# Optimization experiments

Measured on AMD Instinct MI355X. Metric: run time of the kernel, lower is better.

## Reference

```python
import jax, jax.numpy as jnp
import numpy as np
from jax import lax

B, L, D = 2, 2048, 128
H, HD = 8, 32
WIN = 3

def setup_inputs() -> dict:
    key = jax.random.key(0)
    ks = jax.random.split(key, 7)
    s = 0.05
    return {
        "x":  jax.random.normal(ks[0], (B, L, D), jnp.float32),
        "pe": jax.random.normal(ks[1], (L, D), jnp.float32) * s,
        "Wq": jax.random.normal(ks[2], (D, H * HD), jnp.float32) * s,
        "bq": jnp.zeros((H * HD,), jnp.float32),
        "Wk": jax.random.normal(ks[3], (D, H * HD), jnp.float32) * s,
        "bk": jnp.zeros((H * HD,), jnp.float32),
        "Wv": jax.random.normal(ks[4], (D, H), jnp.float32) * s,
    }

def reference(x, pe, Wq, bq, Wk, bk, Wv):
    b, l, d = x.shape
    h = Wv.shape[1]
    hd = Wq.shape[1] // h
    xp = x + pe                                   # (B,L,D)
    # split heads: Dense output columns [i*hd:(i+1)*hd] -> head i
    q = (xp @ Wq + bq).reshape(b, l, h, hd).transpose(2, 0, 1, 3)  # (H,B,L,hd)
    k = (xp @ Wk + bk).reshape(b, l, h, hd).transpose(2, 0, 1, 3)  # (H,B,L,hd)
    v = jax.nn.sigmoid(x @ Wv).transpose(2, 0, 1)                  # (H,B,L)

    attn = jnp.einsum('hbqd,hbkd->hbqk', q, k) * (float(hd) ** -0.5)
    attn = jax.nn.softmax(attn, axis=-1)          # (H,B,L,L)

    # band_part(0,-1) + diag_part(k=(0,L-1)) (RIGHT_LEFT align) + transpose + reverse(-2,-1)
    # collapses to the skew-gather: R[p, m] = attn[L-1-p-m, L-1-p] for p+m <= L-1 else 0
    p = jnp.arange(l)[:, None]                    # (L,1)
    m = jnp.arange(l)[None, :]                    # (1,L)
    ii = l - 1 - p - m                            # row index  (L,L)
    jj = jnp.broadcast_to(l - 1 - p, (l, l))      # col index  (L,L)
    valid = (ii >= 0)
    R = attn[:, :, jnp.where(valid, ii, 0), jj] * valid.astype(attn.dtype)  # (H,B,L,L)

    R = R * v[:, :, :, None]                      # gate by value, broadcast over distance axis

    # TF avg_pool excludes padding from the divisor
    sums = lax.reduce_window(R, 0.0, lax.add, (1, 1, 1, WIN), (1, 1, 1, 1), 'SAME')
    cnt = lax.reduce_window(jnp.ones((l,), R.dtype), 0.0, lax.add, (WIN,), (1,), 'SAME')
    pooled = sums / cnt                           # (H,B,L,L)

    # global mode: sum over position axis, -> (B, L_dist, H)
    out = pooled.sum(axis=2).transpose(1, 2, 0)
    return out
```

## Files before the change

### kernel.cpp

```cpp
#include <hip/hip_runtime.h>
#include <hip/hip_bf16.h>

#define LSEQ 2048
#define BB 2
#define DD 128
#define HH 8
#define HD 32

#define FPSCALE 524288.0f
#define RFPSCALE (1.0f / 524288.0f)
#define QSCALE 0.25503486f

typedef __bf16 bf8_t __attribute__((ext_vector_type(8)));
typedef __bf16 bf4_t __attribute__((ext_vector_type(4)));
typedef float f4_t __attribute__((ext_vector_type(4)));

static __device__ __forceinline__ float fexp2(float x) {
#if __has_builtin(__builtin_amdgcn_exp2f)
    return __builtin_amdgcn_exp2f(x);
#else
    float r;
    asm("v_exp_f32 %0, %1" : "=v"(r) : "v"(x));
    return r;
#endif
}

__global__ __launch_bounds__(256) void k_A(const float* __restrict__ x,
                                           const float* __restrict__ pe,
                                           const float* __restrict__ Wq,
                                           const float* __restrict__ Wk,
                                           const float* __restrict__ Wv,
                                           const float* __restrict__ bq,
                                           const float* __restrict__ bk,
                                           float* __restrict__ w,
                                           __bf16* __restrict__ Qb,
                                           __bf16* __restrict__ Kb,
                                           int* __restrict__ Si) {
    __shared__ __align__(16) char smem[34816];
    int gb = blockIdx.x;
    int tid = threadIdx.x;

    if (gb < 512) {
        __bf16* xs = (__bf16*)smem;
        __bf16* Wt = (__bf16*)(smem + 64 * 136 * 2);
        int jr = gb >> 3, y = gb & 7;
        int row0 = jr * 64;
        bool isK = y >= 4;
        int cbase = (y & 3) * 64;
        const float* W = isK ? Wk : Wq;

        #pragma unroll
        for (int i = 0; i < 8; i++) {
            int idx4 = tid + i * 256;
            int row = idx4 >> 5, col4 = idx4 & 31;
            float4 xv = ((const float4*)x)[row0 * 32 + idx4];
            float4 pv = ((const float4*)pe)[((row0 + row) & (LSEQ - 1)) * 32 + col4];
            bf4_t o = {(__bf16)(xv.x + pv.x), (__bf16)(xv.y + pv.y),
                       (__bf16)(xv.z + pv.z), (__bf16)(xv.w + pv.w)};
            *(bf4_t*)&xs[row * 136 + col4 * 4] = o;
        }
        #pragma unroll
        for (int i = 0; i < 8; i++) {
            int idx4 = tid + i * 256;
            int d = idx4 >> 4, c4 = (idx4 & 15) * 4;
            float4 wv4 = *(const float4*)(W + d * 256 + cbase + c4);
            Wt[(c4 + 0) * 136 + d] = (__bf16)wv4.x;
            Wt[(c4 + 1) * 136 + d] = (__bf16)wv4.y;
            Wt[(c4 + 2) * 136 + d] = (__bf16)wv4.z;
            Wt[(c4 + 3) * 136 + d] = (__bf16)wv4.w;
        }
        __syncthreads();

        int wid = tid >> 6, lane = tid & 63;
        int lm = lane & 15, lq = lane >> 4;
        int c0loc = wid * 16;
        f4_t acc0 = {0,0,0,0}, acc1 = {0,0,0,0}, acc2 = {0,0,0,0}, acc3 = {0,0,0,0};
        #pragma unroll
        for (int s = 0; s < 4; s++) {
            bf8_t bw = *(const bf8_t*)&Wt[(c0loc + lm) * 136 + lq * 8 + s * 32];
            bf8_t a0 = *(const bf8_t*)&xs[(0  + lm) * 136 + lq * 8 + s * 32];
            bf8_t a1 = *(const bf8_t*)&xs[(16 + lm) * 136 + lq * 8 + s * 32];
            bf8_t a2 = *(const bf8_t*)&xs[(32 + lm) * 136 + lq * 8 + s * 32];
            bf8_t a3 = *(const bf8_t*)&xs[(48 + lm) * 136 + lq * 8 + s * 32];
            acc0 = __builtin_amdgcn_mfma_f32_16x16x32_bf16(a0, bw, acc0, 0, 0, 0);
            acc1 = __builtin_amdgcn_mfma_f32_16x16x32_bf16(a1, bw, acc1, 0, 0, 0);
            acc2 = __builtin_amdgcn_mfma_f32_16x16x32_bf16(a2, bw, acc2, 0, 0, 0);
            acc3 = __builtin_amdgcn_mfma_f32_16x16x32_bf16(a3, bw, acc3, 0, 0, 0);
        }
        int c = cbase + c0loc + lm;
        float bv = (isK ? bk : bq)[c];
        float qs = isK ? 1.f : QSCALE;
        __bf16* Out = isK ? Kb : Qb;
        int h = c >> 5, hd = c & 31;
        f4_t accs[4] = {acc0, acc1, acc2, acc3};
        #pragma unroll
        for (int rs = 0; rs < 4; rs++) {
            #pragma unroll
            for (int r = 0; r < 4; r++) {
                int row = row0 + rs * 16 + lq * 4 + r;
                int b_ = row >> 11, l = row & (LSEQ - 1);
                Out[((h * BB + b_) * LSEQ + l) * HD + hd] =
                    (__bf16)((accs[rs][r] + bv) * qs);
            }
        }
    } else if (gb < 640) {
        float* xsf = (float*)smem;
        float* wvf = (float*)(smem + 32 * 132 * 4);
        int r0 = (gb - 512) * 32;
        for (int i = 0; i < 16; i++) {
            int idx = tid + i * 256;
            xsf[(idx >> 7) * 132 + (idx & 127)] = x[r0 * 128 + idx];
        }
        for (int i = 0; i < 4; i++) {
            int idx = tid + i * 256;
            wvf[idx] = Wv[idx];
        }
        __syncthreads();
        int rl = tid >> 3, h = tid & 7;
        float acc = 0.f;
        #pragma unroll 8
        for (int d = 0; d < 128; d++) acc += xsf[rl * 132 + d] * wvf[d * 8 + h];
        float sg = 1.f / (1.f + __expf(-acc));
        int r = r0 + rl;
        int b = r >> 11, l = r & (LSEQ - 1);
        w[(h * BB + b) * LSEQ + (LSEQ - 1 - l)] = sg * FPSCALE;
    } else {
        int4 z = {0, 0, 0, 0};
        ((int4*)Si)[(gb - 640) * 256 + tid] = z;
    }
}

__global__ __launch_bounds__(512) void k_F(const __bf16* __restrict__ Qb,
                                           const __bf16* __restrict__ Kb,
                                           const float* __restrict__ w,
                                           int* __restrict__ S) {
    __shared__ int Sloc[2048];
    __shared__ float dred[128];

    int hb = blockIdx.y;
    int q0 = blockIdx.x << 5;
    int tid = threadIdx.x;
    int wid = tid >> 6, lane = tid & 63;
    int lm = lane & 15, lq = lane >> 4;
    int g = wid >> 2, h = wid & 3;
    int qg0 = q0 + g * 16;

    int4 z4 = {0, 0, 0, 0};
    ((int4*)Sloc)[tid] = z4;

    const __bf16* Qhb = Qb + hb * LSEQ * HD;
    const __bf16* Khb = Kb + hb * LSEQ * HD;
    bf8_t aq = *(const bf8_t*)(Qhb + (qg0 + lm) * HD + lq * 8);

    float dsum[4] = {0.f, 0.f, 0.f, 0.f};
    #pragma unroll 4
    for (int s = h; s < 128; s += 4) {
        bf8_t bk_ = *(const bf8_t*)(Khb + (s * 16 + lm) * HD + lq * 8);
        f4_t z = {0.f, 0.f, 0.f, 0.f};
        f4_t sc = __builtin_amdgcn_mfma_f32_16x16x32_bf16(aq, bk_, z, 0, 0, 0);
        #pragma unroll
        for (int r = 0; r < 4; r++) dsum[r] += fexp2(sc[r]);
    }
    #pragma unroll
    for (int r = 0; r < 4; r++) {
        float v = dsum[r];
        v += __shfl_xor(v, 1);
        v += __shfl_xor(v, 2);
        v += __shfl_xor(v, 4);
        v += __shfl_xor(v, 8);
        dsum[r] = v;
    }
    if (lm == 0) {
        #pragma unroll
        for (int r = 0; r < 4; r++) dred[wid * 16 + lq * 4 + r] = dsum[r];
    }
    __syncthreads();
    float rdv[4];
    #pragma unroll
    for (int r = 0; r < 4; r++) {
        int base = g * 64 + lq * 4 + r;
        float d = dred[base] + dred[base + 16] + dred[base + 32] + dred[base + 48];
        rdv[r] = 1.0f / d;
    }

    const float* whb = w + hb * LSEQ;
    int qrow = qg0 + lq * 4;

    if (h == 0) {
        bf8_t bk_ = *(const bf8_t*)(Khb + (qg0 + lm) * HD + lq * 8);
        f4_t z = {0.f, 0.f, 0.f, 0.f};
        f4_t sc = __builtin_amdgcn_mfma_f32_16x16x32_bf16(aq, bk_, z, 0, 0, 0);
        float wv = whb[qg0 + lm];
        #pragma unroll
        for (int r = 0; r < 4; r++) {
            int m = lm - lq * 4 - r;
            if (m >= 0) {
                int iv = __float2int_rn(fexp2(sc[r]) * rdv[r] * wv);
                atomicAdd(&Sloc[m], iv);
            }
        }
    }
    int nfull = 127 - (qg0 >> 4);
    #pragma unroll 2
    for (int t = h; t < nfull; t += 4) {
        int k0s = qg0 + 16 + t * 16;
        bf8_t bk_ = *(const bf8_t*)(Khb + (k0s + lm) * HD + lq * 8);
        f4_t z = {0.f, 0.f, 0.f, 0.f};
        f4_t sc = __builtin_amdgcn_mfma_f32_16x16x32_bf16(aq, bk_, z, 0, 0, 0);
        float wv = whb[k0s + lm];
        int base = k0s + lm - qrow;
        #pragma unroll
        for (int r = 0; r < 4; r++) {
            int iv = __float2int_rn(fexp2(sc[r]) * rdv[r] * wv);
            atomicAdd(&Sloc[base - r], iv);
        }
    }
    __syncthreads();

    int M = LSEQ - q0;
    int* Sg = S + hb * LSEQ;
    for (int i = tid; i < M; i += 512) {
        int v = Sloc[i];
        if (v) atomicAdd(&Sg[i], v);
    }
}

__global__ __launch_bounds__(256) void k_out(const int* __restrict__ S,
                                             float* __restrict__ out) {
    int idx = blockIdx.x * 256 + threadIdx.x;
    int h = idx & 7;
    int m = (idx >> 3) & (LSEQ - 1);
    int b = idx >> 14;
    const int* Sr = S + (h * BB + b) * LSEQ;
    float s = (float)Sr[m];
    float cnt = 3.f;
    if (m > 0) s += (float)Sr[m - 1]; else cnt = 2.f;
    if (m < LSEQ - 1) s += (float)Sr[m + 1]; else cnt = 2.f;
    out[idx] = s * RFPSCALE / cnt;
}

extern "C" void kernel_launch(void* const* d_in, const int* in_sizes, int n_in,
                              void* d_out, int out_size, void* d_ws, size_t ws_size,
                              hipStream_t stream) {
    const float* x  = (const float*)d_in[0];
    const float* pe = (const float*)d_in[1];
    const float* Wq = (const float*)d_in[2];
    const float* bq = (const float*)d_in[3];
    const float* Wk = (const float*)d_in[4];
    const float* bk = (const float*)d_in[5];
    const float* Wv = (const float*)d_in[6];
    float* out = (float*)d_out;

    char* ws = (char*)d_ws;
    int*    Si  = (int*)(ws);
    float*  w   = (float*)(ws + 131072);
    __bf16* Qb  = (__bf16*)(ws + 262144);
    __bf16* Kb  = (__bf16*)(ws + 262144 + 2097152);

    k_A<<<672, 256, 0, stream>>>(x, pe, Wq, Wk, Wv, bq, bk, w, Qb, Kb, Si);
    k_F<<<dim3(64, 16), 512, 0, stream>>>(Qb, Kb, w, Si);
    k_out<<<128, 256, 0, stream>>>(Si, out);
}
```

Baseline: 113.0 us.

## Fuse output pooling into attention kernel via per-head completion counters

Removes the separate k_out launch. An extra block per head-batch in k_F spin-waits on an atomic counter until all 64 compute blocks for that head have flushed their partial sums, then does the 3-wide pooling and writes the output. This saves one kernel launch and its gap. The cost is a spin-waiting block that occupies a CU slot. The wait can deadlock if the waiting blocks are scheduled before the producers and fill the device, and there is no explicit memory fence around the counter increment.

New measurement: 149.8 us. 1.33x slower.

```diff
diff --git a/kernel.cpp b/kernel.cpp
--- a/kernel.cpp
+++ b/kernel.cpp
@@ -35,7 +35,8 @@
                                            float* __restrict__ w,
                                            __bf16* __restrict__ Qb,
                                            __bf16* __restrict__ Kb,
-                                           int* __restrict__ Si) {
+                                           int* __restrict__ Si,
+                                           int* __restrict__ cnt) {
     __shared__ __align__(16) char smem[34816];
     int gb = blockIdx.x;
     int tid = threadIdx.x;
@@ -124,22 +125,50 @@
         int r = r0 + rl;
         int b = r >> 11, l = r & (LSEQ - 1);
         w[(h * BB + b) * LSEQ + (LSEQ - 1 - l)] = sg * FPSCALE;
-    } else {
+    } else if (gb < 672) {
         int4 z = {0, 0, 0, 0};
         ((int4*)Si)[(gb - 640) * 256 + tid] = z;
+    } else {
+        if (tid < 16) cnt[tid] = 0;
     }
 }
 
 __global__ __launch_bounds__(512) void k_F(const __bf16* __restrict__ Qb,
                                            const __bf16* __restrict__ Kb,
                                            const float* __restrict__ w,
-                                           int* __restrict__ S) {
+                                           int* __restrict__ S,
+                                           int* __restrict__ cnt,
+                                           float* __restrict__ out) {
     __shared__ int Sloc[2048];
     __shared__ float dred[128];
 
     int hb = blockIdx.y;
+    int tid = threadIdx.x;
+
+    if (blockIdx.x == 64) {
+        if (tid == 0) {
+            while (__hip_atomic_load(cnt + hb, __ATOMIC_RELAXED,
+                                     __HIP_MEMORY_SCOPE_AGENT) < 64)
+                __builtin_amdgcn_s_sleep(4);
+        }
+        __syncthreads();
+        const int* Sg = S + hb * LSEQ;
+        for (int m = tid; m < LSEQ; m += 512)
+            Sloc[m] = __hip_atomic_load(Sg + m, __ATOMIC_RELAXED,
+                                        __HIP_MEMORY_SCOPE_AGENT);
+        __syncthreads();
+        int h = hb >> 1, b = hb & 1;
+        for (int m = tid; m < LSEQ; m += 512) {
+            float s = (float)Sloc[m];
+            float c = 3.f;
+            if (m > 0) s += (float)Sloc[m - 1]; else c = 2.f;
+            if (m < LSEQ - 1) s += (float)Sloc[m + 1]; else c = 2.f;
+            out[(b * LSEQ + m) * 8 + h] = s * RFPSCALE / c;
+        }
+        return;
+    }
+
     int q0 = blockIdx.x << 5;
-    int tid = threadIdx.x;
     int wid = tid >> 6, lane = tid & 63;
     int lm = lane & 15, lq = lane >> 4;
     int g = wid >> 2, h = wid & 3;
@@ -223,20 +252,9 @@
         int v = Sloc[i];
         if (v) atomicAdd(&Sg[i], v);
     }
-}
-
-__global__ __launch_bounds__(256) void k_out(const int* __restrict__ S,
-                                             float* __restrict__ out) {
-    int idx = blockIdx.x * 256 + threadIdx.x;
-    int h = idx & 7;
-    int m = (idx >> 3) & (LSEQ - 1);
-    int b = idx >> 14;
-    const int* Sr = S + (h * BB + b) * LSEQ;
-    float s = (float)Sr[m];
-    float cnt = 3.f;
-    if (m > 0) s += (float)Sr[m - 1]; else cnt = 2.f;
-    if (m < LSEQ - 1) s += (float)Sr[m + 1]; else cnt = 2.f;
-    out[idx] = s * RFPSCALE / cnt;
+
+    __syncthreads();
+    if (tid == 0) atomicAdd(&cnt[hb], 1);
 }
 
 extern "C" void kernel_launch(void* const* d_in, const int* in_sizes, int n_in,
@@ -256,8 +274,8 @@
     float*  w   = (float*)(ws + 131072);
     __bf16* Qb  = (__bf16*)(ws + 262144);
     __bf16* Kb  = (__bf16*)(ws + 262144 + 2097152);
-
-    k_A<<<672, 256, 0, stream>>>(x, pe, Wq, Wk, Wv, bq, bk, w, Qb, Kb, Si);
-    k_F<<<dim3(64, 16), 512, 0, stream>>>(Qb, Kb, w, Si);
-    k_out<<<128, 256, 0, stream>>>(Si, out);
-}
+    int*    cnt = (int*)(ws + 262144 + 4194304);
+
+    k_A<<<673, 256, 0, stream>>>(x, pe, Wq, Wk, Wv, bq, bk, w, Qb, Kb, Si, cnt);
+    k_F<<<dim3(65, 16), 512, 0, stream>>>(Qb, Kb, w, Si, cnt, out);
+}
```

## Stage K chunks and gate weights in LDS, double queries per block

Applied to the files above, without the earlier changes.

The attention kernel now copies K in 512-row chunks into shared memory, along with the per-head gate vector, and reads MFMA operands from LDS instead of global memory. Each block handles 64 query rows instead of 32, which halves the grid and raises K reuse per load. The band pass walks the chunks from last to first and stops at the chunk holding the block's diagonal. The cost is extra barriers per chunk, more LDS per block (about 50 KB), and fewer workgroups with only two waves sharing each query tile, which may reduce occupancy and load balance.

Result: faster. 109.9 us (-2.8%).

```diff
diff --git a/kernel.cpp b/kernel.cpp
--- a/kernel.cpp
+++ b/kernel.cpp
@@ -134,15 +134,17 @@
                                            const __bf16* __restrict__ Kb,
                                            const float* __restrict__ w,
                                            int* __restrict__ S) {
-    __shared__ int Sloc[2048];
+    __shared__ __align__(16) __bf16 Kl[512 * HD];
+    __shared__ __align__(16) float  wl[2048];
+    __shared__ __align__(16) int    Sloc[2048];
     __shared__ float dred[128];
 
     int hb = blockIdx.y;
-    int q0 = blockIdx.x << 5;
+    int q0 = blockIdx.x << 6;
     int tid = threadIdx.x;
     int wid = tid >> 6, lane = tid & 63;
     int lm = lane & 15, lq = lane >> 4;
-    int g = wid >> 2, h = wid & 3;
+    int g = wid >> 1, h = wid & 1;
     int qg0 = q0 + g * 16;
 
     int4 z4 = {0, 0, 0, 0};
@@ -150,16 +152,29 @@
 
     const __bf16* Qhb = Qb + hb * LSEQ * HD;
     const __bf16* Khb = Kb + hb * LSEQ * HD;
+
+    ((int4*)wl)[tid] = ((const int4*)(w + hb * LSEQ))[tid];
+
     bf8_t aq = *(const bf8_t*)(Qhb + (qg0 + lm) * HD + lq * 8);
 
     float dsum[4] = {0.f, 0.f, 0.f, 0.f};
-    #pragma unroll 4
-    for (int s = h; s < 128; s += 4) {
-        bf8_t bk_ = *(const bf8_t*)(Khb + (s * 16 + lm) * HD + lq * 8);
-        f4_t z = {0.f, 0.f, 0.f, 0.f};
-        f4_t sc = __builtin_amdgcn_mfma_f32_16x16x32_bf16(aq, bk_, z, 0, 0, 0);
-        #pragma unroll
-        for (int r = 0; r < 4; r++) dsum[r] += fexp2(sc[r]);
+    for (int c = 0; c < 4; c++) {
+        __syncthreads();
+        const int4* gsrc = (const int4*)(Khb + c * 512 * HD);
+        #pragma unroll
+        for (int i = 0; i < 4; i++) {
+            int idx = tid + i * 512;
+            ((int4*)Kl)[idx] = gsrc[idx];
+        }
+        __syncthreads();
+        #pragma unroll 4
+        for (int sl = h; sl < 32; sl += 2) {
+            bf8_t bk_ = *(const bf8_t*)&Kl[(sl * 16 + lm) * HD + lq * 8];
+            f4_t z = {0.f, 0.f, 0.f, 0.f};
+            f4_t sc = __builtin_amdgcn_mfma_f32_16x16x32_bf16(aq, bk_, z, 0, 0, 0);
+            #pragma unroll
+            for (int r = 0; r < 4; r++) dsum[r] += fexp2(sc[r]);
+        }
     }
     #pragma unroll
     for (int r = 0; r < 4; r++) {
@@ -178,41 +193,50 @@
     float rdv[4];
     #pragma unroll
     for (int r = 0; r < 4; r++) {
-        int base = g * 64 + lq * 4 + r;
-        float d = dred[base] + dred[base + 16] + dred[base + 32] + dred[base + 48];
-        rdv[r] = 1.0f / d;
-    }
-
-    const float* whb = w + hb * LSEQ;
+        int base = g * 32 + lq * 4 + r;
+        rdv[r] = 1.0f / (dred[base] + dred[base + 16]);
+    }
+
+    int jb = qg0 >> 4;
+    int c0 = q0 >> 9;
     int qrow = qg0 + lq * 4;
-
-    if (h == 0) {
-        bf8_t bk_ = *(const bf8_t*)(Khb + (qg0 + lm) * HD + lq * 8);
-        f4_t z = {0.f, 0.f, 0.f, 0.f};
-        f4_t sc = __builtin_amdgcn_mfma_f32_16x16x32_bf16(aq, bk_, z, 0, 0, 0);
-        float wv = whb[qg0 + lm];
-        #pragma unroll
-        for (int r = 0; r < 4; r++) {
-            int m = lm - lq * 4 - r;
-            if (m >= 0) {
-                int iv = __float2int_rn(fexp2(sc[r]) * rdv[r] * wv);
-                atomicAdd(&Sloc[m], iv);
+    for (int c = 3; c >= c0; c--) {
+        if (c != 3) {
+            __syncthreads();
+            const int4* gsrc = (const int4*)(Khb + c * 512 * HD);
+            #pragma unroll
+            for (int i = 0; i < 4; i++) {
+                int idx = tid + i * 512;
+                ((int4*)Kl)[idx] = gsrc[idx];
             }
-        }
-    }
-    int nfull = 127 - (qg0 >> 4);
-    #pragma unroll 2
-    for (int t = h; t < nfull; t += 4) {
-        int k0s = qg0 + 16 + t * 16;
-        bf8_t bk_ = *(const bf8_t*)(Khb + (k0s + lm) * HD + lq * 8);
-        f4_t z = {0.f, 0.f, 0.f, 0.f};
-        f4_t sc = __builtin_amdgcn_mfma_f32_16x16x32_bf16(aq, bk_, z, 0, 0, 0);
-        float wv = whb[k0s + lm];
-        int base = k0s + lm - qrow;
-        #pragma unroll
-        for (int r = 0; r < 4; r++) {
-            int iv = __float2int_rn(fexp2(sc[r]) * rdv[r] * wv);
-            atomicAdd(&Sloc[base - r], iv);
+            __syncthreads();
+        }
+        int jlo = jb > c * 32 ? jb : c * 32;
+        int jhi = (c + 1) * 32;
+        int js = jlo + ((jlo ^ h) & 1);
+        for (int j = js; j < jhi; j += 2) {
+            int krow = j * 16 - c * 512 + lm;
+            bf8_t bk_ = *(const bf8_t*)&Kl[krow * HD + lq * 8];
+            f4_t z = {0.f, 0.f, 0.f, 0.f};
+            f4_t sc = __builtin_amdgcn_mfma_f32_16x16x32_bf16(aq, bk_, z, 0, 0, 0);
+            float wv = wl[j * 16 + lm];
+            int base = j * 16 + lm - qrow;
+            if (j == jb) {
+                #pragma unroll
+                for (int r = 0; r < 4; r++) {
+                    int m = base - r;
+                    if (m >= 0) {
+                        int iv = __float2int_rn(fexp2(sc[r]) * rdv[r] * wv);
+                        atomicAdd(&Sloc[m], iv);
+                    }
+                }
+            } else {
+                #pragma unroll
+                for (int r = 0; r < 4; r++) {
+                    int iv = __float2int_rn(fexp2(sc[r]) * rdv[r] * wv);
+                    atomicAdd(&Sloc[base - r], iv);
+                }
+            }
         }
     }
     __syncthreads();
@@ -258,6 +282,6 @@
     __bf16* Kb  = (__bf16*)(ws + 262144 + 2097152);
 
     k_A<<<672, 256, 0, stream>>>(x, pe, Wq, Wk, Wv, bq, bk, w, Qb, Kb, Si);
-    k_F<<<dim3(64, 16), 512, 0, stream>>>(Qb, Kb, w, Si);
+    k_F<<<dim3(32, 16), 512, 0, stream>>>(Qb, Kb, w, Si);
     k_out<<<128, 256, 0, stream>>>(Si, out);
 }
```
